# Performance work log

Measured on AMD Instinct MI355X. Metric: run time of the kernel, lower is better.

Reference implementation:

```python
import jax, jax.numpy as jnp
import numpy as np

EMBED_DIM = 1024
NUM_HEADS = 16
HEAD_DIM = EMBED_DIM // NUM_HEADS
B, S = 8, 1024


def setup_inputs() -> dict:
    key = jax.random.key(0)
    k1, k2, k3, k4, k5 = jax.random.split(key, 5)
    scale_in = 1.0 / np.sqrt(EMBED_DIM)
    return {
        "qkv": jax.random.normal(k1, (B, S, EMBED_DIM), dtype=jnp.float32),
        "w_in": jax.random.normal(k2, (3 * EMBED_DIM, EMBED_DIM), dtype=jnp.float32) * scale_in,
        "b_in": jax.random.normal(k3, (3 * EMBED_DIM,), dtype=jnp.float32) * 0.01,
        "w_out": jax.random.normal(k4, (EMBED_DIM, EMBED_DIM), dtype=jnp.float32) * scale_in,
        "b_out": jax.random.normal(k5, (EMBED_DIM,), dtype=jnp.float32) * 0.01,
    }


def reference(qkv, w_in, b_in, w_out, b_out):
    # in_proj: [B,S,E] -> [B,S,3E]  (torch Linear: x @ W.T + b)
    proj = qkv @ w_in.T + b_in
    q, k, v = jnp.split(proj, 3, axis=2)
    # split heads: [B,S,E] -> [B,S,H,D]
    def heads(t):
        return t.reshape(B, S, NUM_HEADS, HEAD_DIM)
    q, k, v = heads(q), heads(k), heads(v)
    # scaled dot-product attention per head; scale = sqrt(head_dim)
    scores = jnp.einsum("bqhd,bkhd->bhqk", q, k) / jnp.sqrt(jnp.float32(HEAD_DIM))
    attn = jax.nn.softmax(scores, axis=-1)
    out = jnp.einsum("bhqk,bkhd->bqhd", attn, v)  # [B,S,H,D]
    out = out.reshape(B, S, EMBED_DIM)  # concat heads along feature dim
    return out @ w_out.T + b_out
```

## Files before the change

### kernel.cpp

```cpp
#include <hip/hip_runtime.h>

typedef _Float16 f16;
typedef _Float16 f16x4 __attribute__((ext_vector_type(4)));
typedef _Float16 f16x8 __attribute__((ext_vector_type(8)));
typedef float f32x4 __attribute__((ext_vector_type(4)));
typedef float f32x16 __attribute__((ext_vector_type(16)));
typedef unsigned u32x4 __attribute__((ext_vector_type(4)));

#define DEVINL __device__ __forceinline__

DEVINL void gload16(const void* g, void* l) {
    __builtin_amdgcn_global_load_lds(
        (const __attribute__((address_space(1))) unsigned int*)g,
        (__attribute__((address_space(3))) unsigned int*)l, 16, 0, 0);
}

DEVINL unsigned pk2(float a, float b) {
    auto v = __builtin_amdgcn_cvt_pkrtz(a, b);
    return __builtin_bit_cast(unsigned, v);
}

__global__ __launch_bounds__(256) void cvt_kernel(const float* __restrict__ in,
                                                  f16* __restrict__ out, int n4) {
    int i = blockIdx.x * 256 + threadIdx.x;
    int st = gridDim.x * 256;
    for (; i < n4; i += st) {
        float4 v = reinterpret_cast<const float4*>(in)[i];
        f16x4 o = {(f16)v.x, (f16)v.y, (f16)v.z, (f16)v.w};
        reinterpret_cast<f16x4*>(out)[i] = o;
    }
}

template <int EPI>
__global__ __launch_bounds__(256) void gemm_bt(
    const f16* __restrict__ A, const f16* __restrict__ Bm,
    const float* __restrict__ bias, float* __restrict__ Cout,
    f16* __restrict__ Qw, f16* __restrict__ Kw, f16* __restrict__ Vtw) {
    constexpr int K = 1024, NT = K / 32;
    __shared__ f16 As[2][128 * 32];
    __shared__ f16 Bs[2][128 * 32];
    const int t = threadIdx.x;
    const int wave = t >> 6, lane = t & 63, lr = lane & 15, lg = lane >> 4;
    const int wr = wave >> 1, wc = wave & 1;
    const int m0 = blockIdx.y * 128, n0 = blockIdx.x * 128;

    const f16* Ag = A + (m0 + (t >> 2)) * K + (t & 3) * 8;
    const f16* Bg = Bm + (n0 + (t >> 2)) * K + (t & 3) * 8;

    f32x4 acc[4][4] = {};

    auto stage = [&](int buf, int kt) {
        const f16* a = Ag + kt * 32;
        const f16* b = Bg + kt * 32;
        f16* al = &As[buf][t * 8];
        f16* bl = &Bs[buf][t * 8];
        gload16(a, al);
        gload16(a + 64 * K, al + 64 * 32);
        gload16(b, bl);
        gload16(b + 64 * K, bl + 64 * 32);
    };

    stage(0, 0);
    __syncthreads();
    int cur = 0;
    for (int kt = 0; kt < NT; ++kt) {
        if (kt + 1 < NT) stage(cur ^ 1, kt + 1);
        const f16* as = &As[cur][0];
        const f16* bs = &Bs[cur][0];
        f16x8 af[4], bf[4];
#pragma unroll
        for (int i = 0; i < 4; ++i)
            af[i] = *(const f16x8*)&as[(wr * 64 + i * 16 + lr) * 32 + lg * 8];
#pragma unroll
        for (int i = 0; i < 4; ++i)
            bf[i] = *(const f16x8*)&bs[(wc * 64 + i * 16 + lr) * 32 + lg * 8];
#pragma unroll
        for (int i = 0; i < 4; ++i)
#pragma unroll
            for (int j = 0; j < 4; ++j)
                acc[i][j] = __builtin_amdgcn_mfma_f32_16x16x32_f16(af[i], bf[j], acc[i][j], 0, 0, 0);
        __syncthreads();
        cur ^= 1;
    }

    if constexpr (EPI == 0) {
#pragma unroll
        for (int nf = 0; nf < 4; ++nf) {
            int n = n0 + wc * 64 + nf * 16 + lr;
            float bv = bias[n];
            int part = n >> 10, e = n & 1023, hh = e >> 6, dd = e & 63;
#pragma unroll
            for (int mf = 0; mf < 4; ++mf) {
                int m = m0 + wr * 64 + mf * 16 + lg * 4;
                int bb = m >> 10, ss = m & 1023;
                if (part == 0) {
                    f16* dst = Qw + ((bb * 16 + hh) * 1024 + ss) * 64 + dd;
#pragma unroll
                    for (int r = 0; r < 4; ++r) dst[r * 64] = (f16)(acc[mf][nf][r] + bv);
                } else if (part == 1) {
                    f16* dst = Kw + ((bb * 16 + hh) * 1024 + ss) * 64 + dd;
#pragma unroll
                    for (int r = 0; r < 4; ++r) dst[r * 64] = (f16)(acc[mf][nf][r] + bv);
                } else {
                    f16x4 pkv;
#pragma unroll
                    for (int r = 0; r < 4; ++r) pkv[r] = (f16)(acc[mf][nf][r] + bv);
                    *(f16x4*)(Vtw + ((bb * 16 + hh) * 64 + dd) * 1024 + ss) = pkv;
                }
            }
        }
    } else {
#pragma unroll
        for (int nf = 0; nf < 4; ++nf) {
            int n = n0 + wc * 64 + nf * 16 + lr;
            float bv = bias[n];
#pragma unroll
            for (int mf = 0; mf < 4; ++mf) {
                int m = m0 + wr * 64 + mf * 16 + lg * 4;
#pragma unroll
                for (int r = 0; r < 4; ++r) Cout[(m + r) * 1024 + n] = acc[mf][nf][r] + bv;
            }
        }
    }
}

__global__ __launch_bounds__(256) void attn_kernel(const f16* __restrict__ Qw,
                                                   const f16* __restrict__ Kw,
                                                   const f16* __restrict__ Vtw,
                                                   f16* __restrict__ AO) {
    __shared__ f16 Ksm[2][64 * 64];
    __shared__ f16 Vsm[2][64 * 64];
    const int t = threadIdx.x, wave = t >> 6, lane = t & 63;
    const int ql = lane & 31, hi = lane >> 5;
    const int b = blockIdx.z, h = blockIdx.y, qt = blockIdx.x;
    const f16* Qp = Qw + (b * 16 + h) * 1024 * 64;
    const f16* Kp = Kw + (b * 16 + h) * 1024 * 64;
    const f16* Vp = Vtw + (b * 16 + h) * 64 * 1024;
    const int q0 = qt * 128 + wave * 32;

    f16x8 qb[4];
#pragma unroll
    for (int s = 0; s < 4; ++s)
        qb[s] = *(const f16x8*)&Qp[(q0 + ql) * 64 + s * 16 + hi * 8];

    auto stage_kv = [&](int buf, int kv) {
#pragma unroll
        for (int c = 0; c < 2; ++c) {
            int row = c * 32 + (t >> 3);
            int w = (t & 7) << 4;
            int gw = w ^ ((row & 7) << 4);
            gload16((const char*)(Kp + (kv + row) * 64) + gw,
                    (char*)&Ksm[buf][0] + c * 4096 + t * 16);
            gload16((const char*)(Vp + row * 1024 + kv) + gw,
                    (char*)&Vsm[buf][0] + c * 4096 + t * 16);
        }
    };

    f32x16 o0 = 0.f, o1 = 0.f;
    float mraw = -1e30f, lsum = 0.f;
    const float SC = 0.125f * 1.44269504088896f;

    stage_kv(0, 0);
    __syncthreads();
    int cur = 0;

    for (int kv = 0; kv < 16; ++kv) {
        if (kv + 1 < 16) stage_kv(cur ^ 1, (kv + 1) * 64);
        const char* Kb = (const char*)&Ksm[cur][0];
        const char* Vb = (const char*)&Vsm[cur][0];

        f32x16 st0, st1;
#pragma unroll
        for (int s = 0; s < 4; ++s) {
            int r0 = ql, r1 = 32 + ql;
            int byt = (s * 32 + hi * 16) ^ ((r0 & 7) << 4);
            f16x8 k0 = *(const f16x8*)(Kb + r0 * 128 + byt);
            f16x8 k1 = *(const f16x8*)(Kb + r1 * 128 + byt);
            if (s == 0) {
                st0 = __builtin_amdgcn_mfma_f32_32x32x16_f16(k0, qb[0], (f32x16)0.f, 0, 0, 0);
                st1 = __builtin_amdgcn_mfma_f32_32x32x16_f16(k1, qb[0], (f32x16)0.f, 0, 0, 0);
            } else {
                st0 = __builtin_amdgcn_mfma_f32_32x32x16_f16(k0, qb[s], st0, 0, 0, 0);
                st1 = __builtin_amdgcn_mfma_f32_32x32x16_f16(k1, qb[s], st1, 0, 0, 0);
            }
        }

        float mx = st0[0];
#pragma unroll
        for (int r = 1; r < 16; ++r) mx = fmaxf(mx, st0[r]);
#pragma unroll
        for (int r = 0; r < 16; ++r) mx = fmaxf(mx, st1[r]);
        mx = fmaxf(mx, __shfl_xor(mx, 32, 64));
        float mn = fmaxf(mraw, mx);
        float al = exp2f((mraw - mn) * SC);
        mraw = mn;
        float msc = mn * SC;
        float ps = 0.f;
#pragma unroll
        for (int r = 0; r < 16; ++r) {
            float p = exp2f(fmaf(st0[r], SC, -msc));
            st0[r] = p;
            ps += p;
        }
#pragma unroll
        for (int r = 0; r < 16; ++r) {
            float p = exp2f(fmaf(st1[r], SC, -msc));
            st1[r] = p;
            ps += p;
        }
        ps += __shfl_xor(ps, 32, 64);
        lsum = lsum * al + ps;
        o0 *= al;
        o1 *= al;

#pragma unroll
        for (int s = 0; s < 4; ++s) {
            const int s1 = s & 1;
            float p0, p1, p2, p3, p4, p5, p6, p7;
            if (s < 2) {
                p0 = st0[8 * s1 + 0]; p1 = st0[8 * s1 + 1]; p2 = st0[8 * s1 + 2]; p3 = st0[8 * s1 + 3];
                p4 = st0[8 * s1 + 4]; p5 = st0[8 * s1 + 5]; p6 = st0[8 * s1 + 6]; p7 = st0[8 * s1 + 7];
            } else {
                p0 = st1[8 * s1 + 0]; p1 = st1[8 * s1 + 1]; p2 = st1[8 * s1 + 2]; p3 = st1[8 * s1 + 3];
                p4 = st1[8 * s1 + 4]; p5 = st1[8 * s1 + 5]; p6 = st1[8 * s1 + 6]; p7 = st1[8 * s1 + 7];
            }
            unsigned c0 = pk2(p0, p1), c1 = pk2(p2, p3);
            unsigned c2 = pk2(p4, p5), c3 = pk2(p6, p7);
            unsigned y0 = __shfl_xor(hi ? c0 : c2, 32, 64);
            unsigned y1 = __shfl_xor(hi ? c1 : c3, 32, 64);
            unsigned w0 = hi ? y0 : c0;
            unsigned w1 = hi ? y1 : c1;
            unsigned w2 = hi ? c2 : y0;
            unsigned w3 = hi ? c3 : y1;
            u32x4 pw = {w0, w1, w2, w3};
            f16x8 pf = __builtin_bit_cast(f16x8, pw);
#pragma unroll
            for (int db = 0; db < 2; ++db) {
                int row = db * 32 + ql;
                int byt = (s * 32 + hi * 16) ^ ((row & 7) << 4);
                f16x8 vf = *(const f16x8*)(Vb + row * 128 + byt);
                if (db == 0)
                    o0 = __builtin_amdgcn_mfma_f32_32x32x16_f16(vf, pf, o0, 0, 0, 0);
                else
                    o1 = __builtin_amdgcn_mfma_f32_32x32x16_f16(vf, pf, o1, 0, 0, 0);
            }
        }
        __syncthreads();
        cur ^= 1;
    }

    float inv = 1.0f / lsum;
    char* obase = (char*)&Ksm[0][0] + wave * 4096;
#pragma unroll
    for (int db = 0; db < 2; ++db)
#pragma unroll
        for (int r = 0; r < 16; ++r) {
            int d = db * 32 + (r & 3) + 8 * (r >> 2) + 4 * hi;
            float v = (db == 0 ? o0[r] : o1[r]) * inv;
            *(f16*)(obase + ql * 128 + ((2 * d) ^ ((ql & 7) << 4))) = (f16)v;
        }
    __syncthreads();
    const int rl = lane >> 1, c4 = (lane & 1) * 4;
#pragma unroll
    for (int i = 0; i < 4; ++i) {
        f16x8 ov = *(const f16x8*)(obase + rl * 128 + (((c4 + i) * 16) ^ ((rl & 7) << 4)));
        *(f16x8*)&AO[(b * 1024 + q0 + rl) * 1024 + h * 64 + (c4 + i) * 8] = ov;
    }
}

extern "C" void kernel_launch(void* const* d_in, const int* in_sizes, int n_in,
                              void* d_out, int out_size, void* d_ws, size_t ws_size,
                              hipStream_t stream) {
    const float* qkv = (const float*)d_in[0];
    const float* w_in = (const float*)d_in[1];
    const float* b_in = (const float*)d_in[2];
    const float* w_out = (const float*)d_in[3];
    const float* b_out = (const float*)d_in[4];
    float* out = (float*)d_out;

    f16* Xh = (f16*)d_ws;
    f16* Wih = Xh + 8388608;
    f16* Woh = Wih + 3145728;
    f16* Qw = Woh + 1048576;
    f16* Kw = Qw + 8388608;
    f16* Vtw = Kw + 8388608;
    f16* AO = Xh;

    cvt_kernel<<<2048, 256, 0, stream>>>(qkv, Xh, 8388608 / 4);
    cvt_kernel<<<1024, 256, 0, stream>>>(w_in, Wih, 3145728 / 4);
    cvt_kernel<<<512, 256, 0, stream>>>(w_out, Woh, 1048576 / 4);

    gemm_bt<0><<<dim3(24, 64), 256, 0, stream>>>(Xh, Wih, b_in, nullptr, Qw, Kw, Vtw);
    attn_kernel<<<dim3(8, 16, 8), 256, 0, stream>>>(Qw, Kw, Vtw, AO);
    gemm_bt<1><<<dim3(8, 64), 256, 0, stream>>>(AO, Woh, b_out, out, nullptr, nullptr, nullptr);
}
```

Baseline: 298.7 us.

## Deepen LDS pipelines, enlarge in-proj GEMM tile, add lazy softmax rescale

The QKV projection becomes a 512-thread kernel with a 128x384 tile, a 4-slot LDS ring buffer, XOR-swizzled LDS layout, explicit vmcnt waits and raised MFMA priority. The softmax scale and log2e are folded into Q during the projection epilogue. Attention moves from 2 to 4 KV buffers with a 3-deep prefetch and raw barriers, and skips rescaling the O accumulators when the running max grows by at most 8 (log2 units). These changes aim to hide global load latency and trim exp and VALU work, at the cost of more LDS use, lower occupancy, and a less precise fp16 Q scaled before rounding.

```diff
diff --git a/kernel.cpp b/kernel.cpp
--- a/kernel.cpp
+++ b/kernel.cpp
@@ -8,6 +8,7 @@
 typedef unsigned u32x4 __attribute__((ext_vector_type(4)));
 
 #define DEVINL __device__ __forceinline__
+#define VMCNT(n) asm volatile("s_waitcnt vmcnt(" #n ")" ::: "memory")
 
 DEVINL void gload16(const void* g, void* l) {
     __builtin_amdgcn_global_load_lds(
@@ -31,11 +32,108 @@
     }
 }
 
-template <int EPI>
-__global__ __launch_bounds__(256) void gemm_bt(
-    const f16* __restrict__ A, const f16* __restrict__ Bm,
-    const float* __restrict__ bias, float* __restrict__ Cout,
-    f16* __restrict__ Qw, f16* __restrict__ Kw, f16* __restrict__ Vtw) {
+__global__ __launch_bounds__(512) void gemm_in(const f16* __restrict__ A,
+                                               const f16* __restrict__ Bm,
+                                               const float* __restrict__ bias,
+                                               f16* __restrict__ Qw, f16* __restrict__ Kw,
+                                               f16* __restrict__ Vtw) {
+    constexpr int NKT = 32;
+    __shared__ f16 As[4][128 * 32];
+    __shared__ f16 Bs[4][384 * 32];
+    const int t = threadIdx.x;
+    const int w = t >> 6, lane = t & 63, lr = lane & 15, lg = lane >> 4;
+    const int wm = w >> 2, wn = w & 3;
+    const int m0 = blockIdx.y * 128, n0 = blockIdx.x * 384;
+
+    const int srow = t >> 2, scol = (t & 3) * 16;
+    const char* Asrc = (const char*)(A + (m0 + srow) * 1024) + (scol ^ (((srow >> 1) & 3) << 4));
+    const char* Bsrc[3];
+#pragma unroll
+    for (int r = 0; r < 3; ++r) {
+        int row = r * 128 + srow;
+        Bsrc[r] = (const char*)(Bm + (n0 + row) * 1024) + (scol ^ (((row >> 1) & 3) << 4));
+    }
+
+    auto stage = [&](int buf, int kt) {
+        gload16(Asrc + kt * 64, (char*)&As[buf][0] + t * 16);
+#pragma unroll
+        for (int r = 0; r < 3; ++r)
+            gload16(Bsrc[r] + kt * 64, (char*)&Bs[buf][0] + r * 8192 + t * 16);
+    };
+
+    int offA[4], offB[6];
+#pragma unroll
+    for (int mf = 0; mf < 4; ++mf) {
+        int row = wm * 64 + mf * 16 + lr;
+        offA[mf] = row * 64 + ((lg * 16) ^ (((row >> 1) & 3) << 4));
+    }
+#pragma unroll
+    for (int nf = 0; nf < 6; ++nf) {
+        int row = wn * 96 + nf * 16 + lr;
+        offB[nf] = row * 64 + ((lg * 16) ^ (((row >> 1) & 3) << 4));
+    }
+
+    f32x4 acc[4][6] = {};
+
+    stage(0, 0);
+    stage(1, 1);
+    stage(2, 2);
+    VMCNT(8);
+
+    for (int kt = 0; kt < NKT; ++kt) {
+        __builtin_amdgcn_s_barrier();
+        if (kt + 3 < NKT) stage((kt + 3) & 3, kt + 3);
+        const char* ab = (const char*)&As[kt & 3][0];
+        const char* bb = (const char*)&Bs[kt & 3][0];
+        f16x8 af[4], bf[6];
+#pragma unroll
+        for (int mf = 0; mf < 4; ++mf) af[mf] = *(const f16x8*)(ab + offA[mf]);
+#pragma unroll
+        for (int nf = 0; nf < 6; ++nf) bf[nf] = *(const f16x8*)(bb + offB[nf]);
+        __builtin_amdgcn_s_setprio(1);
+#pragma unroll
+        for (int mf = 0; mf < 4; ++mf)
+#pragma unroll
+            for (int nf = 0; nf < 6; ++nf)
+                acc[mf][nf] = __builtin_amdgcn_mfma_f32_16x16x32_f16(af[mf], bf[nf], acc[mf][nf], 0, 0, 0);
+        __builtin_amdgcn_s_setprio(0);
+        if (kt <= NKT - 4) VMCNT(8);
+        else if (kt == NKT - 3) VMCNT(4);
+        else if (kt == NKT - 2) VMCNT(0);
+    }
+
+    const float SCQ = 0.18033688011112042f;
+#pragma unroll
+    for (int nf = 0; nf < 6; ++nf) {
+        int n = n0 + wn * 96 + nf * 16 + lr;
+        float bv = bias[n];
+        int part = n >> 10, e = n & 1023, hh = e >> 6, dd = e & 63;
+#pragma unroll
+        for (int mf = 0; mf < 4; ++mf) {
+            int m = m0 + wm * 64 + mf * 16 + lg * 4;
+            int bb2 = m >> 10, ss = m & 1023;
+            if (part == 0) {
+                f16* dst = Qw + ((bb2 * 16 + hh) * 1024 + ss) * 64 + dd;
+#pragma unroll
+                for (int r = 0; r < 4; ++r) dst[r * 64] = (f16)((acc[mf][nf][r] + bv) * SCQ);
+            } else if (part == 1) {
+                f16* dst = Kw + ((bb2 * 16 + hh) * 1024 + ss) * 64 + dd;
+#pragma unroll
+                for (int r = 0; r < 4; ++r) dst[r * 64] = (f16)(acc[mf][nf][r] + bv);
+            } else {
+                f16x4 pkv;
+#pragma unroll
+                for (int r = 0; r < 4; ++r) pkv[r] = (f16)(acc[mf][nf][r] + bv);
+                *(f16x4*)(Vtw + ((bb2 * 16 + hh) * 64 + dd) * 1024 + ss) = pkv;
+            }
+        }
+    }
+}
+
+__global__ __launch_bounds__(256) void gemm_out(const f16* __restrict__ A,
+                                                const f16* __restrict__ Bm,
+                                                const float* __restrict__ bias,
+                                                float* __restrict__ Cout) {
     constexpr int K = 1024, NT = K / 32;
     __shared__ f16 As[2][128 * 32];
     __shared__ f16 Bs[2][128 * 32];
@@ -82,44 +180,15 @@
         __syncthreads();
         cur ^= 1;
     }
-
-    if constexpr (EPI == 0) {
-#pragma unroll
-        for (int nf = 0; nf < 4; ++nf) {
-            int n = n0 + wc * 64 + nf * 16 + lr;
-            float bv = bias[n];
-            int part = n >> 10, e = n & 1023, hh = e >> 6, dd = e & 63;
-#pragma unroll
-            for (int mf = 0; mf < 4; ++mf) {
-                int m = m0 + wr * 64 + mf * 16 + lg * 4;
-                int bb = m >> 10, ss = m & 1023;
-                if (part == 0) {
-                    f16* dst = Qw + ((bb * 16 + hh) * 1024 + ss) * 64 + dd;
-#pragma unroll
-                    for (int r = 0; r < 4; ++r) dst[r * 64] = (f16)(acc[mf][nf][r] + bv);
-                } else if (part == 1) {
-                    f16* dst = Kw + ((bb * 16 + hh) * 1024 + ss) * 64 + dd;
-#pragma unroll
-                    for (int r = 0; r < 4; ++r) dst[r * 64] = (f16)(acc[mf][nf][r] + bv);
-                } else {
-                    f16x4 pkv;
-#pragma unroll
-                    for (int r = 0; r < 4; ++r) pkv[r] = (f16)(acc[mf][nf][r] + bv);
-                    *(f16x4*)(Vtw + ((bb * 16 + hh) * 64 + dd) * 1024 + ss) = pkv;
-                }
-            }
-        }
-    } else {
-#pragma unroll
-        for (int nf = 0; nf < 4; ++nf) {
-            int n = n0 + wc * 64 + nf * 16 + lr;
-            float bv = bias[n];
-#pragma unroll
-            for (int mf = 0; mf < 4; ++mf) {
-                int m = m0 + wr * 64 + mf * 16 + lg * 4;
-#pragma unroll
-                for (int r = 0; r < 4; ++r) Cout[(m + r) * 1024 + n] = acc[mf][nf][r] + bv;
-            }
+#pragma unroll
+    for (int nf = 0; nf < 4; ++nf) {
+        int n = n0 + wc * 64 + nf * 16 + lr;
+        float bv = bias[n];
+#pragma unroll
+        for (int mf = 0; mf < 4; ++mf) {
+            int m = m0 + wr * 64 + mf * 16 + lg * 4;
+#pragma unroll
+            for (int r = 0; r < 4; ++r) Cout[(m + r) * 1024 + n] = acc[mf][nf][r] + bv;
         }
     }
 }
@@ -128,8 +197,8 @@
                                                    const f16* __restrict__ Kw,
                                                    const f16* __restrict__ Vtw,
                                                    f16* __restrict__ AO) {
-    __shared__ f16 Ksm[2][64 * 64];
-    __shared__ f16 Vsm[2][64 * 64];
+    __shared__ f16 Ksm[4][64 * 64];
+    __shared__ f16 Vsm[4][64 * 64];
     const int t = threadIdx.x, wave = t >> 6, lane = t & 63;
     const int ql = lane & 31, hi = lane >> 5;
     const int b = blockIdx.z, h = blockIdx.y, qt = blockIdx.x;
@@ -143,33 +212,36 @@
     for (int s = 0; s < 4; ++s)
         qb[s] = *(const f16x8*)&Qp[(q0 + ql) * 64 + s * 16 + hi * 8];
 
-    auto stage_kv = [&](int buf, int kv) {
+    const int srow0 = t >> 3;
+    const int sw = ((t & 7) << 4);
+    auto stage_kv = [&](int slot, int kv) {
 #pragma unroll
         for (int c = 0; c < 2; ++c) {
-            int row = c * 32 + (t >> 3);
-            int w = (t & 7) << 4;
-            int gw = w ^ ((row & 7) << 4);
+            int row = c * 32 + srow0;
+            int gw = sw ^ ((row & 7) << 4);
             gload16((const char*)(Kp + (kv + row) * 64) + gw,
-                    (char*)&Ksm[buf][0] + c * 4096 + t * 16);
+                    (char*)&Ksm[slot][0] + c * 4096 + t * 16);
             gload16((const char*)(Vp + row * 1024 + kv) + gw,
-                    (char*)&Vsm[buf][0] + c * 4096 + t * 16);
+                    (char*)&Vsm[slot][0] + c * 4096 + t * 16);
         }
     };
 
     f32x16 o0 = 0.f, o1 = 0.f;
     float mraw = -1e30f, lsum = 0.f;
-    const float SC = 0.125f * 1.44269504088896f;
 
     stage_kv(0, 0);
-    __syncthreads();
-    int cur = 0;
+    stage_kv(1, 64);
+    stage_kv(2, 128);
+    VMCNT(8);
 
     for (int kv = 0; kv < 16; ++kv) {
-        if (kv + 1 < 16) stage_kv(cur ^ 1, (kv + 1) * 64);
-        const char* Kb = (const char*)&Ksm[cur][0];
-        const char* Vb = (const char*)&Vsm[cur][0];
+        __builtin_amdgcn_s_barrier();
+        if (kv + 3 < 16) stage_kv((kv + 3) & 3, (kv + 3) * 64);
+        const char* Kb = (const char*)&Ksm[kv & 3][0];
+        const char* Vb = (const char*)&Vsm[kv & 3][0];
 
         f32x16 st0, st1;
+        __builtin_amdgcn_s_setprio(1);
 #pragma unroll
         for (int s = 0; s < 4; ++s) {
             int r0 = ql, r1 = 32 + ql;
@@ -184,6 +256,7 @@
                 st1 = __builtin_amdgcn_mfma_f32_32x32x16_f16(k1, qb[s], st1, 0, 0, 0);
             }
         }
+        __builtin_amdgcn_s_setprio(0);
 
         float mx = st0[0];
 #pragma unroll
@@ -191,27 +264,45 @@
 #pragma unroll
         for (int r = 0; r < 16; ++r) mx = fmaxf(mx, st1[r]);
         mx = fmaxf(mx, __shfl_xor(mx, 32, 64));
-        float mn = fmaxf(mraw, mx);
-        float al = exp2f((mraw - mn) * SC);
-        mraw = mn;
-        float msc = mn * SC;
-        float ps = 0.f;
-#pragma unroll
-        for (int r = 0; r < 16; ++r) {
-            float p = exp2f(fmaf(st0[r], SC, -msc));
-            st0[r] = p;
-            ps += p;
-        }
-#pragma unroll
-        for (int r = 0; r < 16; ++r) {
-            float p = exp2f(fmaf(st1[r], SC, -msc));
-            st1[r] = p;
-            ps += p;
-        }
-        ps += __shfl_xor(ps, 32, 64);
-        lsum = lsum * al + ps;
-        o0 *= al;
-        o1 *= al;
+
+        if (__all(mx <= mraw + 8.f)) {
+            float ps = 0.f;
+#pragma unroll
+            for (int r = 0; r < 16; ++r) {
+                float p = exp2f(st0[r] - mraw);
+                st0[r] = p;
+                ps += p;
+            }
+#pragma unroll
+            for (int r = 0; r < 16; ++r) {
+                float p = exp2f(st1[r] - mraw);
+                st1[r] = p;
+                ps += p;
+            }
+            ps += __shfl_xor(ps, 32, 64);
+            lsum += ps;
+        } else {
+            float mn = fmaxf(mraw, mx);
+            float al = exp2f(mraw - mn);
+            mraw = mn;
+            float ps = 0.f;
+#pragma unroll
+            for (int r = 0; r < 16; ++r) {
+                float p = exp2f(st0[r] - mn);
+                st0[r] = p;
+                ps += p;
+            }
+#pragma unroll
+            for (int r = 0; r < 16; ++r) {
+                float p = exp2f(st1[r] - mn);
+                st1[r] = p;
+                ps += p;
+            }
+            ps += __shfl_xor(ps, 32, 64);
+            lsum = lsum * al + ps;
+            o0 *= al;
+            o1 *= al;
+        }
 
 #pragma unroll
         for (int s = 0; s < 4; ++s) {
@@ -234,6 +325,7 @@
             unsigned w3 = hi ? c3 : y1;
             u32x4 pw = {w0, w1, w2, w3};
             f16x8 pf = __builtin_bit_cast(f16x8, pw);
+            __builtin_amdgcn_s_setprio(1);
 #pragma unroll
             for (int db = 0; db < 2; ++db) {
                 int row = db * 32 + ql;
@@ -244,9 +336,11 @@
                 else
                     o1 = __builtin_amdgcn_mfma_f32_32x32x16_f16(vf, pf, o1, 0, 0, 0);
             }
-        }
-        __syncthreads();
-        cur ^= 1;
+            __builtin_amdgcn_s_setprio(0);
+        }
+        if (kv <= 12) VMCNT(8);
+        else if (kv == 13) VMCNT(4);
+        else if (kv == 14) VMCNT(0);
     }
 
     float inv = 1.0f / lsum;
@@ -290,7 +384,7 @@
     cvt_kernel<<<1024, 256, 0, stream>>>(w_in, Wih, 3145728 / 4);
     cvt_kernel<<<512, 256, 0, stream>>>(w_out, Woh, 1048576 / 4);
 
-    gemm_bt<0><<<dim3(24, 64), 256, 0, stream>>>(Xh, Wih, b_in, nullptr, Qw, Kw, Vtw);
+    gemm_in<<<dim3(8, 64), 512, 0, stream>>>(Xh, Wih, b_in, Qw, Kw, Vtw);
     attn_kernel<<<dim3(8, 16, 8), 256, 0, stream>>>(Qw, Kw, Vtw, AO);
-    gemm_bt<1><<<dim3(8, 64), 256, 0, stream>>>(AO, Woh, b_out, out, nullptr, nullptr, nullptr);
-}
+    gemm_out<<<dim3(8, 64), 256, 0, stream>>>(AO, Woh, b_out, out);
+}
```

After: 304.3 us. About the same (+1.9%).

## Deepen attention KV pipeline, fold softmax scale into Q, add lazy rescaling

Applied to the files above, without the earlier changes.

The attention kernel now uses 512-thread blocks covering 256 queries and a 4-slot LDS ring. It prefetches three KV tiles ahead, waiting with explicit vmcnt counts and a raw barrier instead of a full __syncthreads per tile. The softmax scale and log2e factor are folded into Q in the input-projection epilogue. Softmax uses tree reductions and skips rescaling the output accumulators unless the running max grows by more than 8 (log2 units); s_setprio is raised around MFMA sections. The GEMM template is split into two separate kernels. Risks include fp16 range of the scaled Q, correctness of the hand-counted vmcnt/barrier ordering, and occupancy with 64KB of LDS per block.

```diff
diff --git a/kernel.cpp b/kernel.cpp
--- a/kernel.cpp
+++ b/kernel.cpp
@@ -8,6 +8,7 @@
 typedef unsigned u32x4 __attribute__((ext_vector_type(4)));
 
 #define DEVINL __device__ __forceinline__
+#define VMCNT(n) asm volatile("s_waitcnt vmcnt(" #n ")" ::: "memory")
 
 DEVINL void gload16(const void* g, void* l) {
     __builtin_amdgcn_global_load_lds(
@@ -31,11 +32,11 @@
     }
 }
 
-template <int EPI>
-__global__ __launch_bounds__(256) void gemm_bt(
-    const f16* __restrict__ A, const f16* __restrict__ Bm,
-    const float* __restrict__ bias, float* __restrict__ Cout,
-    f16* __restrict__ Qw, f16* __restrict__ Kw, f16* __restrict__ Vtw) {
+__global__ __launch_bounds__(256) void gemm_in(const f16* __restrict__ A,
+                                               const f16* __restrict__ Bm,
+                                               const float* __restrict__ bias,
+                                               f16* __restrict__ Qw, f16* __restrict__ Kw,
+                                               f16* __restrict__ Vtw) {
     constexpr int K = 1024, NT = K / 32;
     __shared__ f16 As[2][128 * 32];
     __shared__ f16 Bs[2][128 * 32];
@@ -83,99 +84,143 @@
         cur ^= 1;
     }
 
-    if constexpr (EPI == 0) {
-#pragma unroll
-        for (int nf = 0; nf < 4; ++nf) {
-            int n = n0 + wc * 64 + nf * 16 + lr;
-            float bv = bias[n];
-            int part = n >> 10, e = n & 1023, hh = e >> 6, dd = e & 63;
-#pragma unroll
-            for (int mf = 0; mf < 4; ++mf) {
-                int m = m0 + wr * 64 + mf * 16 + lg * 4;
-                int bb = m >> 10, ss = m & 1023;
-                if (part == 0) {
-                    f16* dst = Qw + ((bb * 16 + hh) * 1024 + ss) * 64 + dd;
-#pragma unroll
-                    for (int r = 0; r < 4; ++r) dst[r * 64] = (f16)(acc[mf][nf][r] + bv);
-                } else if (part == 1) {
-                    f16* dst = Kw + ((bb * 16 + hh) * 1024 + ss) * 64 + dd;
-#pragma unroll
-                    for (int r = 0; r < 4; ++r) dst[r * 64] = (f16)(acc[mf][nf][r] + bv);
-                } else {
-                    f16x4 pkv;
-#pragma unroll
-                    for (int r = 0; r < 4; ++r) pkv[r] = (f16)(acc[mf][nf][r] + bv);
-                    *(f16x4*)(Vtw + ((bb * 16 + hh) * 64 + dd) * 1024 + ss) = pkv;
-                }
+    const float SCQ = 0.18033688011112042f;
+#pragma unroll
+    for (int nf = 0; nf < 4; ++nf) {
+        int n = n0 + wc * 64 + nf * 16 + lr;
+        float bv = bias[n];
+        int part = n >> 10, e = n & 1023, hh = e >> 6, dd = e & 63;
+#pragma unroll
+        for (int mf = 0; mf < 4; ++mf) {
+            int m = m0 + wr * 64 + mf * 16 + lg * 4;
+            int bb = m >> 10, ss = m & 1023;
+            if (part == 0) {
+                f16* dst = Qw + ((bb * 16 + hh) * 1024 + ss) * 64 + dd;
+#pragma unroll
+                for (int r = 0; r < 4; ++r) dst[r * 64] = (f16)((acc[mf][nf][r] + bv) * SCQ);
+            } else if (part == 1) {
+                f16* dst = Kw + ((bb * 16 + hh) * 1024 + ss) * 64 + dd;
+#pragma unroll
+                for (int r = 0; r < 4; ++r) dst[r * 64] = (f16)(acc[mf][nf][r] + bv);
+            } else {
+                f16x4 pkv;
+#pragma unroll
+                for (int r = 0; r < 4; ++r) pkv[r] = (f16)(acc[mf][nf][r] + bv);
+                *(f16x4*)(Vtw + ((bb * 16 + hh) * 64 + dd) * 1024 + ss) = pkv;
             }
         }
-    } else {
-#pragma unroll
-        for (int nf = 0; nf < 4; ++nf) {
-            int n = n0 + wc * 64 + nf * 16 + lr;
-            float bv = bias[n];
-#pragma unroll
-            for (int mf = 0; mf < 4; ++mf) {
-                int m = m0 + wr * 64 + mf * 16 + lg * 4;
-#pragma unroll
-                for (int r = 0; r < 4; ++r) Cout[(m + r) * 1024 + n] = acc[mf][nf][r] + bv;
-            }
-        }
-    }
-}
-
-__global__ __launch_bounds__(256) void attn_kernel(const f16* __restrict__ Qw,
-                                                   const f16* __restrict__ Kw,
-                                                   const f16* __restrict__ Vtw,
-                                                   f16* __restrict__ AO) {
-    __shared__ f16 Ksm[2][64 * 64];
-    __shared__ f16 Vsm[2][64 * 64];
+    }
+}
+
+__global__ __launch_bounds__(256) void gemm_out(const f16* __restrict__ A,
+                                                const f16* __restrict__ Bm,
+                                                const float* __restrict__ bias,
+                                                float* __restrict__ Cout) {
+    constexpr int K = 1024, NT = K / 32;
+    __shared__ f16 As[2][128 * 32];
+    __shared__ f16 Bs[2][128 * 32];
+    const int t = threadIdx.x;
+    const int wave = t >> 6, lane = t & 63, lr = lane & 15, lg = lane >> 4;
+    const int wr = wave >> 1, wc = wave & 1;
+    const int m0 = blockIdx.y * 128, n0 = blockIdx.x * 128;
+
+    const f16* Ag = A + (m0 + (t >> 2)) * K + (t & 3) * 8;
+    const f16* Bg = Bm + (n0 + (t >> 2)) * K + (t & 3) * 8;
+
+    f32x4 acc[4][4] = {};
+
+    auto stage = [&](int buf, int kt) {
+        const f16* a = Ag + kt * 32;
+        const f16* b = Bg + kt * 32;
+        f16* al = &As[buf][t * 8];
+        f16* bl = &Bs[buf][t * 8];
+        gload16(a, al);
+        gload16(a + 64 * K, al + 64 * 32);
+        gload16(b, bl);
+        gload16(b + 64 * K, bl + 64 * 32);
+    };
+
+    stage(0, 0);
+    __syncthreads();
+    int cur = 0;
+    for (int kt = 0; kt < NT; ++kt) {
+        if (kt + 1 < NT) stage(cur ^ 1, kt + 1);
+        const f16* as = &As[cur][0];
+        const f16* bs = &Bs[cur][0];
+        f16x8 af[4], bf[4];
+#pragma unroll
+        for (int i = 0; i < 4; ++i)
+            af[i] = *(const f16x8*)&as[(wr * 64 + i * 16 + lr) * 32 + lg * 8];
+#pragma unroll
+        for (int i = 0; i < 4; ++i)
+            bf[i] = *(const f16x8*)&bs[(wc * 64 + i * 16 + lr) * 32 + lg * 8];
+#pragma unroll
+        for (int i = 0; i < 4; ++i)
+#pragma unroll
+            for (int j = 0; j < 4; ++j)
+                acc[i][j] = __builtin_amdgcn_mfma_f32_16x16x32_f16(af[i], bf[j], acc[i][j], 0, 0, 0);
+        __syncthreads();
+        cur ^= 1;
+    }
+#pragma unroll
+    for (int nf = 0; nf < 4; ++nf) {
+        int n = n0 + wc * 64 + nf * 16 + lr;
+        float bv = bias[n];
+#pragma unroll
+        for (int mf = 0; mf < 4; ++mf) {
+            int m = m0 + wr * 64 + mf * 16 + lg * 4;
+#pragma unroll
+            for (int r = 0; r < 4; ++r) Cout[(m + r) * 1024 + n] = acc[mf][nf][r] + bv;
+        }
+    }
+}
+
+__global__ __launch_bounds__(512, 4) void attn_kernel(const f16* __restrict__ Qw,
+                                                      const f16* __restrict__ Kw,
+                                                      const f16* __restrict__ Vtw,
+                                                      f16* __restrict__ AO) {
+    __shared__ char LDSb[65536];
     const int t = threadIdx.x, wave = t >> 6, lane = t & 63;
     const int ql = lane & 31, hi = lane >> 5;
     const int b = blockIdx.z, h = blockIdx.y, qt = blockIdx.x;
     const f16* Qp = Qw + (b * 16 + h) * 1024 * 64;
     const f16* Kp = Kw + (b * 16 + h) * 1024 * 64;
     const f16* Vp = Vtw + (b * 16 + h) * 64 * 1024;
-    const int q0 = qt * 128 + wave * 32;
+    const int q0 = qt * 256 + wave * 32;
 
     f16x8 qb[4];
 #pragma unroll
     for (int s = 0; s < 4; ++s)
         qb[s] = *(const f16x8*)&Qp[(q0 + ql) * 64 + s * 16 + hi * 8];
 
-    auto stage_kv = [&](int buf, int kv) {
-#pragma unroll
-        for (int c = 0; c < 2; ++c) {
-            int row = c * 32 + (t >> 3);
-            int w = (t & 7) << 4;
-            int gw = w ^ ((row & 7) << 4);
-            gload16((const char*)(Kp + (kv + row) * 64) + gw,
-                    (char*)&Ksm[buf][0] + c * 4096 + t * 16);
-            gload16((const char*)(Vp + row * 1024 + kv) + gw,
-                    (char*)&Vsm[buf][0] + c * 4096 + t * 16);
-        }
+    const int srow = t >> 3;
+    const int gw = ((t & 7) << 4) ^ ((srow & 7) << 4);
+    auto stage_kv = [&](int slot, int kv) {
+        gload16((const char*)(Kp + (kv + srow) * 64) + gw, LDSb + slot * 8192 + t * 16);
+        gload16((const char*)(Vp + srow * 1024 + kv) + gw, LDSb + 32768 + slot * 8192 + t * 16);
     };
 
     f32x16 o0 = 0.f, o1 = 0.f;
     float mraw = -1e30f, lsum = 0.f;
-    const float SC = 0.125f * 1.44269504088896f;
 
     stage_kv(0, 0);
-    __syncthreads();
-    int cur = 0;
+    stage_kv(1, 64);
+    stage_kv(2, 128);
+    VMCNT(4);
 
     for (int kv = 0; kv < 16; ++kv) {
-        if (kv + 1 < 16) stage_kv(cur ^ 1, (kv + 1) * 64);
-        const char* Kb = (const char*)&Ksm[cur][0];
-        const char* Vb = (const char*)&Vsm[cur][0];
+        __builtin_amdgcn_s_barrier();
+        if (kv + 3 < 16) stage_kv((kv + 3) & 3, (kv + 3) * 64);
+        const char* Kb = LDSb + (kv & 3) * 8192;
+        const char* Vb = LDSb + 32768 + (kv & 3) * 8192;
 
         f32x16 st0, st1;
+        __builtin_amdgcn_s_setprio(1);
 #pragma unroll
         for (int s = 0; s < 4; ++s) {
-            int r0 = ql, r1 = 32 + ql;
-            int byt = (s * 32 + hi * 16) ^ ((r0 & 7) << 4);
-            f16x8 k0 = *(const f16x8*)(Kb + r0 * 128 + byt);
-            f16x8 k1 = *(const f16x8*)(Kb + r1 * 128 + byt);
+            int byt = (s * 32 + hi * 16) ^ ((ql & 7) << 4);
+            f16x8 k0 = *(const f16x8*)(Kb + ql * 128 + byt);
+            f16x8 k1 = *(const f16x8*)(Kb + (32 + ql) * 128 + byt);
             if (s == 0) {
                 st0 = __builtin_amdgcn_mfma_f32_32x32x16_f16(k0, qb[0], (f32x16)0.f, 0, 0, 0);
                 st1 = __builtin_amdgcn_mfma_f32_32x32x16_f16(k1, qb[0], (f32x16)0.f, 0, 0, 0);
@@ -184,34 +229,52 @@
                 st1 = __builtin_amdgcn_mfma_f32_32x32x16_f16(k1, qb[s], st1, 0, 0, 0);
             }
         }
-
-        float mx = st0[0];
-#pragma unroll
-        for (int r = 1; r < 16; ++r) mx = fmaxf(mx, st0[r]);
-#pragma unroll
-        for (int r = 0; r < 16; ++r) mx = fmaxf(mx, st1[r]);
-        mx = fmaxf(mx, __shfl_xor(mx, 32, 64));
-        float mn = fmaxf(mraw, mx);
-        float al = exp2f((mraw - mn) * SC);
-        mraw = mn;
-        float msc = mn * SC;
-        float ps = 0.f;
-#pragma unroll
-        for (int r = 0; r < 16; ++r) {
-            float p = exp2f(fmaf(st0[r], SC, -msc));
-            st0[r] = p;
-            ps += p;
-        }
-#pragma unroll
-        for (int r = 0; r < 16; ++r) {
-            float p = exp2f(fmaf(st1[r], SC, -msc));
-            st1[r] = p;
-            ps += p;
-        }
-        ps += __shfl_xor(ps, 32, 64);
-        lsum = lsum * al + ps;
-        o0 *= al;
-        o1 *= al;
+        __builtin_amdgcn_s_setprio(0);
+
+        float a[16];
+#pragma unroll
+        for (int r = 0; r < 16; ++r) a[r] = fmaxf(st0[r], st1[r]);
+#pragma unroll
+        for (int s = 8; s >= 1; s >>= 1)
+#pragma unroll
+            for (int r = 0; r < 16; ++r)
+                if (r < s) a[r] = fmaxf(a[r], a[r + s]);
+        float mx = fmaxf(a[0], __shfl_xor(a[0], 32, 64));
+
+        if (__all(mx <= mraw + 8.f)) {
+#pragma unroll
+            for (int r = 0; r < 16; ++r) st0[r] = exp2f(st0[r] - mraw);
+#pragma unroll
+            for (int r = 0; r < 16; ++r) st1[r] = exp2f(st1[r] - mraw);
+            float sa[16];
+#pragma unroll
+            for (int r = 0; r < 16; ++r) sa[r] = st0[r] + st1[r];
+#pragma unroll
+            for (int s = 8; s >= 1; s >>= 1)
+#pragma unroll
+                for (int r = 0; r < 16; ++r)
+                    if (r < s) sa[r] += sa[r + s];
+            lsum += sa[0] + __shfl_xor(sa[0], 32, 64);
+        } else {
+            float mn = fmaxf(mraw, mx);
+            float al = exp2f(mraw - mn);
+            mraw = mn;
+#pragma unroll
+            for (int r = 0; r < 16; ++r) st0[r] = exp2f(st0[r] - mn);
+#pragma unroll
+            for (int r = 0; r < 16; ++r) st1[r] = exp2f(st1[r] - mn);
+            float sa[16];
+#pragma unroll
+            for (int r = 0; r < 16; ++r) sa[r] = st0[r] + st1[r];
+#pragma unroll
+            for (int s = 8; s >= 1; s >>= 1)
+#pragma unroll
+                for (int r = 0; r < 16; ++r)
+                    if (r < s) sa[r] += sa[r + s];
+            lsum = lsum * al + sa[0] + __shfl_xor(sa[0], 32, 64);
+            o0 *= al;
+            o1 *= al;
+        }
 
 #pragma unroll
         for (int s = 0; s < 4; ++s) {
@@ -234,6 +297,7 @@
             unsigned w3 = hi ? c3 : y1;
             u32x4 pw = {w0, w1, w2, w3};
             f16x8 pf = __builtin_bit_cast(f16x8, pw);
+            __builtin_amdgcn_s_setprio(1);
 #pragma unroll
             for (int db = 0; db < 2; ++db) {
                 int row = db * 32 + ql;
@@ -244,13 +308,16 @@
                 else
                     o1 = __builtin_amdgcn_mfma_f32_32x32x16_f16(vf, pf, o1, 0, 0, 0);
             }
-        }
-        __syncthreads();
-        cur ^= 1;
-    }
-
+            __builtin_amdgcn_s_setprio(0);
+        }
+        if (kv <= 12) VMCNT(4);
+        else if (kv == 13) VMCNT(2);
+        else if (kv == 14) VMCNT(0);
+    }
+
+    __syncthreads();
     float inv = 1.0f / lsum;
-    char* obase = (char*)&Ksm[0][0] + wave * 4096;
+    char* obase = LDSb + wave * 4096;
 #pragma unroll
     for (int db = 0; db < 2; ++db)
 #pragma unroll
@@ -290,7 +357,7 @@
     cvt_kernel<<<1024, 256, 0, stream>>>(w_in, Wih, 3145728 / 4);
     cvt_kernel<<<512, 256, 0, stream>>>(w_out, Woh, 1048576 / 4);
 
-    gemm_bt<0><<<dim3(24, 64), 256, 0, stream>>>(Xh, Wih, b_in, nullptr, Qw, Kw, Vtw);
-    attn_kernel<<<dim3(8, 16, 8), 256, 0, stream>>>(Qw, Kw, Vtw, AO);
-    gemm_bt<1><<<dim3(8, 64), 256, 0, stream>>>(AO, Woh, b_out, out, nullptr, nullptr, nullptr);
-}
+    gemm_in<<<dim3(24, 64), 256, 0, stream>>>(Xh, Wih, b_in, Qw, Kw, Vtw);
+    attn_kernel<<<dim3(4, 16, 8), 512, 0, stream>>>(Qw, Kw, Vtw, AO);
+    gemm_out<<<dim3(8, 64), 256, 0, stream>>>(AO, Woh, b_out, out);
+}
```

After: 381.3 us. 27.7% more time.
